# Performance work log

Hardware: AMD Instinct MI355X
Metric: run time of the kernel (lower is better)

Reference implementation:

```python
import jax, jax.numpy as jnp
import numpy as np

D_MODEL = 1024
NUM_HEADS = 16
DEPTH = D_MODEL // NUM_HEADS


def setup_inputs() -> dict:
    key = jax.random.key(0)
    ks = jax.random.split(key, 13)
    B, S = 4, 2048
    s = 1.0 / np.sqrt(D_MODEL)
    return {
        "query": jax.random.normal(ks[0], (B, S, D_MODEL), jnp.float32),
        "key": jax.random.normal(ks[1], (B, S, D_MODEL), jnp.float32),
        "value": jax.random.normal(ks[2], (B, S, D_MODEL), jnp.float32),
        "mask": jax.random.uniform(ks[3], (B, 1, 1, S), jnp.float32),
        "Wq": jax.random.normal(ks[4], (D_MODEL, D_MODEL), jnp.float32) * s,
        "bq": jnp.zeros((D_MODEL,), jnp.float32),
        "Wk": jax.random.normal(ks[5], (D_MODEL, D_MODEL), jnp.float32) * s,
        "bk": jnp.zeros((D_MODEL,), jnp.float32),
        "Wv": jax.random.normal(ks[6], (D_MODEL, D_MODEL), jnp.float32) * s,
        "bv": jnp.zeros((D_MODEL,), jnp.float32),
        "Wo": jax.random.normal(ks[7], (D_MODEL, D_MODEL), jnp.float32) * s,
        "bo": jnp.zeros((D_MODEL,), jnp.float32),
    }


def _split_heads(x):
    # [B, S, d_model] -> [B, H, S, depth]
    B, S, _ = x.shape
    return x.reshape(B, S, NUM_HEADS, DEPTH).transpose(0, 2, 1, 3)


def reference(query, key, value, mask, Wq, bq, Wk, bk, Wv, bv, Wo, bo):
    q = _split_heads(query @ Wq + bq)   # [B,H,Sq,dh]
    k = _split_heads(key @ Wk + bk)     # [B,H,Sk,dh]
    v = _split_heads(value @ Wv + bv)   # [B,H,Sk,dh]
    scale = 1.0 / jnp.sqrt(jnp.float32(DEPTH))
    scores = jnp.einsum("bhqd,bhkd->bhqk", q, k) * scale
    scores = scores + mask * -1e9
    attn = jax.nn.softmax(scores, axis=-1)
    out = jnp.einsum("bhqk,bhkd->bhqd", attn, v)  # [B,H,Sq,dh]
    B, _, Sq, _ = out.shape
    concat = out.transpose(0, 2, 1, 3).reshape(B, Sq, D_MODEL)
    return concat @ Wo + bo
```

## Files before the change

kernel.cpp:

```cpp
#include <hip/hip_runtime.h>

typedef unsigned short ushort_t;
typedef __attribute__((ext_vector_type(8))) short short8;
typedef __attribute__((ext_vector_type(4))) float f32x4;
typedef __attribute__((ext_vector_type(16))) float f32x16;
typedef __attribute__((ext_vector_type(2))) unsigned int uint2v;
typedef __attribute__((ext_vector_type(4))) unsigned int uint4v;
typedef __attribute__((ext_vector_type(2))) unsigned int uint2s;

typedef __attribute__((address_space(1))) const unsigned char gaddr_t;
typedef __attribute__((address_space(3))) unsigned char laddr_t;

__device__ __forceinline__ unsigned short f2bf(float x) {
  unsigned u = __float_as_uint(x);
  u += 0x7FFF + ((u >> 16) & 1);
  return (unsigned short)(u >> 16);
}
__device__ __forceinline__ float bf2f(unsigned short u) {
  return __uint_as_float(((unsigned)u) << 16);
}
__device__ __forceinline__ unsigned cvt_pk_bf16(float lo, float hi) {
  unsigned r;
  asm("v_cvt_pk_bf16_f32 %0, %1, %2" : "=v"(r) : "v"(lo), "v"(hi));
  return r;
}

__device__ __forceinline__ void gl_lds16(const void* g, void* l) {
  __builtin_amdgcn_global_load_lds((gaddr_t*)g, (laddr_t*)l, 16, 0, 0);
}

__device__ __forceinline__ unsigned active_mask(const float* __restrict__ tb) {
  unsigned am = 0;
  float run = -INFINITY;
#pragma unroll
  for (int tt = 0; tt < 32; tt++) {
    float tm = tb[tt];
    if (tm > run - 40.f) am |= (1u << tt);
    run = fmaxf(run, tm);
  }
  return am;
}

__global__ void prep0(const float* __restrict__ maskin, float* __restrict__ maskpre,
                      float* __restrict__ tmaxbuf) {
  const float CM = -1.442695041e9f;
  int bx = blockIdx.x;
  if (bx < 8) {
    int i = bx * 1024 + threadIdx.x * 4;
    f32x4 v = *(const f32x4*)(maskin + i);
    v *= CM;
    *(f32x4*)(maskpre + i) = v;
  } else {
    int t = threadIdx.x;
    if (t < 128) {
      const float* src = maskin + (t >> 5) * 2048 + (t & 31) * 64;
      float mn = src[0];
#pragma unroll
      for (int j = 1; j < 64; j++) mn = fminf(mn, src[j]);
      tmaxbuf[t] = mn * CM;
    }
  }
}

__global__ void prep1(const float4* __restrict__ q4, const float4* __restrict__ k4,
                      const float4* __restrict__ v4,
                      ushort4* __restrict__ xq, ushort4* __restrict__ xk,
                      ushort4* __restrict__ xv,
                      const float* __restrict__ W0, const float* __restrict__ W1,
                      const float* __restrict__ W2, const float* __restrict__ W3,
                      ushort_t* __restrict__ T0, ushort_t* __restrict__ T1,
                      ushort_t* __restrict__ T2, ushort_t* __restrict__ T3,
                      const float* __restrict__ tmaxbuf) {
  const int K = 1024, N = 1024;
  __shared__ ushort_t tile[32][33];
  int bx = blockIdx.x;
  if (bx < 3072) {
    int z = bx >> 10, bl = bx & 1023;
    if (z > 0) {
      int b = bl >> 8, tl = (bl >> 3) & 31;
      unsigned am = active_mask(tmaxbuf + b * 32);
      if (!((am >> tl) & 1u)) return;
    }
    const float4* in = (z == 0) ? q4 : (z == 1) ? k4 : v4;
    ushort4* out = (z == 0) ? xq : (z == 1) ? xk : xv;
    const float4* src = in + (long)bl * 2048;
    ushort4* dst = out + (long)bl * 2048;
    int t = threadIdx.x;
#pragma unroll
    for (int j = 0; j < 8; j++) {
      int idx = j * 256 + t;
      float4 v = src[idx];
      ushort4 o;
      o.x = f2bf(v.x); o.y = f2bf(v.y); o.z = f2bf(v.z); o.w = f2bf(v.w);
      dst[idx] = o;
    }
  } else {
    int idx = bx - 3072;
    int z = idx >> 10;
    const float* W = (z == 0) ? W0 : (z == 1) ? W1 : (z == 2) ? W2 : W3;
    ushort_t* Wt = (z == 0) ? T0 : (z == 1) ? T1 : (z == 2) ? T2 : T3;
    int n0 = (idx & 31) * 32, k0 = ((idx >> 5) & 31) * 32;
    int tx = threadIdx.x & 31, ty = threadIdx.x >> 5;
#pragma unroll
    for (int r = 0; r < 4; r++) {
      int k = k0 + ty + r * 8;
      tile[ty + r * 8][tx] = f2bf(W[(long)k * N + n0 + tx]);
    }
    __syncthreads();
#pragma unroll
    for (int r = 0; r < 4; r++) {
      int n = n0 + ty + r * 8;
      Wt[(long)n * K + k0 + tx] = tile[tx][ty + r * 8];
    }
  }
}

__global__ void gemm_qkv3(
    const ushort_t* __restrict__ Aq, const ushort_t* __restrict__ Ak, const ushort_t* __restrict__ Av,
    const ushort_t* __restrict__ Bq, const ushort_t* __restrict__ Bk, const ushort_t* __restrict__ Bv,
    const float* __restrict__ bq, const float* __restrict__ bk, const float* __restrict__ bv,
    ushort_t* __restrict__ Cq, ushort_t* __restrict__ Ck, ushort_t* __restrict__ Vt,
    const float* __restrict__ tmaxbuf) {
  const int K = 1024, N = 1024;
  const int z = blockIdx.z;
  const ushort_t* A = z == 0 ? Aq : z == 1 ? Ak : Av;
  const ushort_t* Bt = z == 0 ? Bq : z == 1 ? Bk : Bv;
  const float* bias = z == 0 ? bq : z == 1 ? bk : bv;

  __shared__ __align__(16) char smem[49152];
  const int t = threadIdx.x, w = t >> 6, l = t & 63;

  const int orig = blockIdx.x + gridDim.x * blockIdx.y;
  const int xcd = orig & 7, i = orig >> 3;
  const int m0 = (xcd * 8 + (i & 7)) * 128;
  const int n0 = (i >> 3) * 128;
  const int wr = (w >> 1) * 64, wc = (w & 1) * 64;

  if (z != 0) {
    int b_ = m0 >> 11, tile0 = (m0 & 2047) >> 6;
    unsigned am = active_mask(tmaxbuf + b_ * 32);
    if (!((am >> tile0) & 3u)) return;
  }

  f32x4 acc[4][4] = {};

  const int br0 = 16 * w + (l >> 2);
  const int bcs = ((l & 3) ^ ((l >> 3) & 3)) << 3;
  const ushort_t* Ab = A + (long)m0 * K;
  const ushort_t* Bb = Bt + (long)n0 * K;

  auto stage = [&](int kk, int buf) {
    char* base = smem + buf * 16384;
    gl_lds16(Ab + (long)br0 * K + kk + bcs, base + w * 1024);
    gl_lds16(Ab + (long)(br0 + 64) * K + kk + bcs, base + 4096 + w * 1024);
    gl_lds16(Bb + (long)br0 * K + kk + bcs, base + 8192 + w * 1024);
    gl_lds16(Bb + (long)(br0 + 64) * K + kk + bcs, base + 12288 + w * 1024);
  };

  stage(0, 0);
  stage(32, 1);

  const int fsw = ((l >> 4) ^ ((l >> 1) & 3)) << 4;
  const int arow = (wr + (l & 15)) * 64 + fsw;
  const int brow = 8192 + (wc + (l & 15)) * 64 + fsw;

  asm volatile("s_waitcnt vmcnt(4)");
  __builtin_amdgcn_sched_barrier(0);
  __builtin_amdgcn_s_barrier();

  for (int ts = 0; ts < 32; ts++) {
    const char* base = smem + (ts % 3) * 16384;
    if (ts + 2 < 32) stage((ts + 2) * 32, (ts + 2) % 3);
    short8 af[4], bfr[4];
#pragma unroll
    for (int m = 0; m < 4; m++)
      af[m] = *(const short8*)(base + arow + m * 1024);
#pragma unroll
    for (int n = 0; n < 4; n++)
      bfr[n] = *(const short8*)(base + brow + n * 1024);
    __builtin_amdgcn_s_setprio(1);
#pragma unroll
    for (int m = 0; m < 4; m++)
#pragma unroll
      for (int n = 0; n < 4; n++)
        acc[m][n] = __builtin_amdgcn_mfma_f32_16x16x32_bf16(af[m], bfr[n], acc[m][n], 0, 0, 0);
    __builtin_amdgcn_s_setprio(0);
    if (ts < 30) asm volatile("s_waitcnt vmcnt(4)");
    else if (ts == 30) asm volatile("s_waitcnt vmcnt(0)");
    if (ts < 31) {
      __builtin_amdgcn_sched_barrier(0);
      __builtin_amdgcn_s_barrier();
    }
  }
  __builtin_amdgcn_s_barrier();

  char* Lw = smem + w * 8192;
  if (z != 2) {
#pragma unroll
    for (int nn = 0; nn < 4; nn++) {
      float bvv = bias[n0 + wc + nn * 16 + (l & 15)];
      int dl = nn * 16 + (l & 15);
#pragma unroll
      for (int mm = 0; mm < 4; mm++)
#pragma unroll
        for (int i2 = 0; i2 < 4; i2++) {
          int sl = mm * 16 + (l >> 4) * 4 + i2;
          *(ushort_t*)(Lw + sl * 128 + ((dl * 2) ^ ((sl & 7) << 4))) =
              f2bf(acc[mm][nn][i2] + bvv);
        }
    }
    ushort_t* C = (z == 0 ? Cq : Ck) + (long)(m0 + wr) * N + n0 + wc;
#pragma unroll
    for (int rr = 0; rr < 8; rr++) {
      int sl = rr * 8 + (l >> 3);
      short8 vv = *(const short8*)(Lw + sl * 128 + (((l & 7) * 16) ^ ((sl & 7) << 4)));
      *(short8*)(C + (long)sl * N + (l & 7) * 8) = vv;
    }
  } else {
#pragma unroll
    for (int nn = 0; nn < 4; nn++) {
      float bvv = bias[n0 + wc + nn * 16 + (l & 15)];
      int dl = nn * 16 + (l & 15);
#pragma unroll
      for (int mm = 0; mm < 4; mm++) {
        int sl = mm * 16 + (l >> 4) * 4;
        uint2s pk;
        pk.x = cvt_pk_bf16(acc[mm][nn][0] + bvv, acc[mm][nn][1] + bvv);
        pk.y = cvt_pk_bf16(acc[mm][nn][2] + bvv, acc[mm][nn][3] + bvv);
        *(uint2s*)(Lw + dl * 128 + ((sl * 2) ^ ((dl & 7) << 4))) = pk;
      }
    }
    const int b_ = m0 >> 11;
    const int s0g = (m0 & 2047) + wr;
#pragma unroll
    for (int rr = 0; rr < 8; rr++) {
      int dl = rr * 8 + (l >> 3);
      short8 vv = *(const short8*)(Lw + dl * 128 + (((l & 7) * 16) ^ ((dl & 7) << 4)));
      int dg = n0 + wc + dl;
      long rowbase = ((long)(b_ * 16 + (dg >> 6)) * 64 + (dg & 63)) * 2048;
      *(short8*)(Vt + rowbase + s0g + (l & 7) * 8) = vv;
    }
  }
}

__global__ void gemm_o(const ushort_t* __restrict__ A, const ushort_t* __restrict__ Bt,
                       const float* __restrict__ bias, float* __restrict__ C) {
  const int K = 1024, N = 1024;
  __shared__ __align__(16) char smem[49152];
  const int t = threadIdx.x, w = t >> 6, l = t & 63;

  const int orig = blockIdx.x + gridDim.x * blockIdx.y;
  const int xcd = orig & 7, i = orig >> 3;
  const int m0 = (xcd * 8 + (i & 7)) * 128;
  const int n0 = (i >> 3) * 128;
  const int wr = (w >> 1) * 64, wc = (w & 1) * 64;

  f32x4 acc[4][4] = {};

  const int br0 = 16 * w + (l >> 2);
  const int bcs = ((l & 3) ^ ((l >> 3) & 3)) << 3;
  const ushort_t* Ab = A + (long)m0 * K;
  const ushort_t* Bb = Bt + (long)n0 * K;

  auto stage = [&](int kk, int buf) {
    char* base = smem + buf * 16384;
    gl_lds16(Ab + (long)br0 * K + kk + bcs, base + w * 1024);
    gl_lds16(Ab + (long)(br0 + 64) * K + kk + bcs, base + 4096 + w * 1024);
    gl_lds16(Bb + (long)br0 * K + kk + bcs, base + 8192 + w * 1024);
    gl_lds16(Bb + (long)(br0 + 64) * K + kk + bcs, base + 12288 + w * 1024);
  };

  stage(0, 0);
  stage(32, 1);

  const int fsw = ((l >> 4) ^ ((l >> 1) & 3)) << 4;
  const int arow = (wr + (l & 15)) * 64 + fsw;
  const int brow = 8192 + (wc + (l & 15)) * 64 + fsw;

  asm volatile("s_waitcnt vmcnt(4)");
  __builtin_amdgcn_sched_barrier(0);
  __builtin_amdgcn_s_barrier();

  for (int ts = 0; ts < 32; ts++) {
    const char* base = smem + (ts % 3) * 16384;
    if (ts + 2 < 32) stage((ts + 2) * 32, (ts + 2) % 3);
    short8 af[4], bfr[4];
#pragma unroll
    for (int m = 0; m < 4; m++)
      af[m] = *(const short8*)(base + arow + m * 1024);
#pragma unroll
    for (int n = 0; n < 4; n++)
      bfr[n] = *(const short8*)(base + brow + n * 1024);
    __builtin_amdgcn_s_setprio(1);
#pragma unroll
    for (int m = 0; m < 4; m++)
#pragma unroll
      for (int n = 0; n < 4; n++)
        acc[m][n] = __builtin_amdgcn_mfma_f32_16x16x32_bf16(af[m], bfr[n], acc[m][n], 0, 0, 0);
    __builtin_amdgcn_s_setprio(0);
    if (ts < 30) asm volatile("s_waitcnt vmcnt(4)");
    else if (ts == 30) asm volatile("s_waitcnt vmcnt(0)");
    if (ts < 31) {
      __builtin_amdgcn_sched_barrier(0);
      __builtin_amdgcn_s_barrier();
    }
  }

#pragma unroll
  for (int mm = 0; mm < 4; mm++)
#pragma unroll
    for (int nn = 0; nn < 4; nn++) {
      int c = n0 + wc + nn * 16 + (l & 15);
      float bv = bias[c];
#pragma unroll
      for (int i2 = 0; i2 < 4; i2++) {
        int r = m0 + wr + mm * 16 + (l >> 4) * 4 + i2;
        C[(long)r * N + c] = acc[mm][nn][i2] + bv;
      }
    }
}

__global__ __launch_bounds__(256, 4) void attn(
    const ushort_t* __restrict__ Qp, const ushort_t* __restrict__ Kp,
    const ushort_t* __restrict__ Vt, const float* __restrict__ maskpre,
    const float* __restrict__ tmaxbuf, ushort_t* __restrict__ Ob) {
  const int S = 2048, DM = 1024;
  __shared__ __align__(16) char smem[32768];
  char* KlB = smem;
  char* VlB = smem + 16384;

  const int t = threadIdx.x, w = t >> 6, l = t & 63;
  const int lq = l & 31, hi = l >> 5;
  const int hib = hi * 16;

  const int orig = blockIdx.x + (blockIdx.y << 4) + (blockIdx.z << 8);
  const int work = ((orig & 7) << 7) + (orig >> 3);
  const int qx = work & 15;
  const int hb = work >> 4;
  const int h = hb & 15, b = hb >> 4;
  const int q0w = qx * 128 + w * 32;

  const float C1 = 0.1803368801f;

  const ushort_t* Kbase = Kp + (long)(b * S) * DM + h * 64;
  const ushort_t* Vbase = Vt + (long)((b * 16 + h) * 64) * S;
  const float* Mbase = maskpre + (long)b * S;

  short8 qB[4];
  {
    const ushort_t* Qb = Qp + ((long)(b * S) + q0w + lq) * DM + h * 64;
#pragma unroll
    for (int kh = 0; kh < 4; kh++)
      qB[kh] = *(const short8*)(Qb + kh * 16 + hi * 8);
  }

  const int so0 = w * 2048 + l * 16;
  const int sr0 = so0 >> 7, sc0 = (so0 & 127) ^ ((sr0 & 7) << 4);
  const int so1 = so0 + 1024;
  const int sr1 = so1 >> 7, sc1 = (so1 & 127) ^ ((sr1 & 7) << 4);
  const ushort_t* Kg0 = Kbase + (long)sr0 * DM + (sc0 >> 1);
  const ushort_t* Kg1 = Kbase + (long)sr1 * DM + (sc1 >> 1);
  const ushort_t* Vg0 = Vbase + (long)sr0 * S + (sc0 >> 1);
  const ushort_t* Vg1 = Vbase + (long)sr1 * S + (sc1 >> 1);
  char* Kd0 = KlB + w * 2048;
  char* Vd0 = VlB + w * 2048;

  auto stage = [&](int kv0, int bb) {
    long ko = (long)kv0 * DM;
    int bo = bb * 8192;
    gl_lds16(Kg0 + ko, Kd0 + bo);
    gl_lds16(Kg1 + ko, Kd0 + bo + 1024);
    gl_lds16(Vg0 + kv0, Vd0 + bo);
    gl_lds16(Vg1 + kv0, Vd0 + bo + 1024);
  };

  unsigned amask = active_mask(tmaxbuf + b * 32);

  int cur = (int)__builtin_ctz(amask);
  stage(cur * 64, 0);
  __syncthreads();

  const int lbase = lq * 128 + ((lq & 7) << 4);

  f32x16 o0 = {}, o1 = {};
  float mrun = -INFINITY, lsum = 0.f;
  int bb = 0;

  while (cur >= 0) {
    unsigned rem = amask & (0xFFFFFFFEu << cur);
    int nxt = rem ? (int)__builtin_ctz(rem) : -1;
    if (nxt >= 0) stage(nxt * 64, bb ^ 1);
    const int bx = lbase + (bb << 13);
    const int kv0 = cur * 64;

    f32x16 s0 = {}, s1 = {};
    __builtin_amdgcn_s_setprio(1);
#pragma unroll
    for (int kh = 0; kh < 4; kh++) {
      int a = bx ^ (kh * 32 + hib);
      short8 ka0 = *(const short8*)(KlB + a);
      short8 ka1 = *(const short8*)(KlB + a + 4096);
      s0 = __builtin_amdgcn_mfma_f32_32x32x16_bf16(ka0, qB[kh], s0, 0, 0, 0);
      s1 = __builtin_amdgcn_mfma_f32_32x32x16_bf16(ka1, qB[kh], s1, 0, 0, 0);
    }
    __builtin_amdgcn_s_setprio(0);

    const float* mq = Mbase + kv0;
#pragma unroll
    for (int g = 0; g < 4; g++) {
      f32x4 m0 = *(const f32x4*)(mq + g * 8 + hi * 4);
      f32x4 m1 = *(const f32x4*)(mq + 32 + g * 8 + hi * 4);
#pragma unroll
      for (int c = 0; c < 4; c++) {
        s0[g * 4 + c] = fmaf(s0[g * 4 + c], C1, m0[c]);
        s1[g * 4 + c] = fmaf(s1[g * 4 + c], C1, m1[c]);
      }
    }

    float mx0 = -INFINITY, mx1 = -INFINITY, mx2 = -INFINITY, mx3 = -INFINITY;
#pragma unroll
    for (int r = 0; r < 4; r++) {
      mx0 = fmaxf(mx0, fmaxf(s0[r], s0[r + 4]));
      mx1 = fmaxf(mx1, fmaxf(s0[r + 8], s0[r + 12]));
      mx2 = fmaxf(mx2, fmaxf(s1[r], s1[r + 4]));
      mx3 = fmaxf(mx3, fmaxf(s1[r + 8], s1[r + 12]));
    }
    float mx = fmaxf(fmaxf(mx0, mx1), fmaxf(mx2, mx3));
    mx = fmaxf(mx, __shfl_xor(mx, 32));

    if (!__all((int)(mx <= mrun + 8.f))) {
      float mnew = fmaxf(mrun, mx);
      float sc = __builtin_amdgcn_exp2f(mrun - mnew);
      mrun = mnew;
      lsum *= sc;
#pragma unroll
      for (int r = 0; r < 16; r++) { o0[r] *= sc; o1[r] *= sc; }
    }

    float ps0 = 0.f, ps1 = 0.f, ps2 = 0.f, ps3 = 0.f;
#pragma unroll
    for (int r = 0; r < 8; r++) {
      float p0 = __builtin_amdgcn_exp2f(s0[r] - mrun);
      float p1 = __builtin_amdgcn_exp2f(s0[r + 8] - mrun);
      float p2 = __builtin_amdgcn_exp2f(s1[r] - mrun);
      float p3 = __builtin_amdgcn_exp2f(s1[r + 8] - mrun);
      s0[r] = p0; s0[r + 8] = p1; s1[r] = p2; s1[r + 8] = p3;
      ps0 += p0; ps1 += p1; ps2 += p2; ps3 += p3;
    }
    float ps = (ps0 + ps1) + (ps2 + ps3);
    ps += __shfl_xor(ps, 32);
    lsum += ps;

#pragma unroll
    for (int half = 0; half < 2; half++) {
      const f32x16& sv = half ? s1 : s0;
      unsigned x0 = cvt_pk_bf16(sv[0], sv[1]);
      unsigned z0 = cvt_pk_bf16(sv[2], sv[3]);
      unsigned y0 = cvt_pk_bf16(sv[4], sv[5]);
      unsigned u0 = cvt_pk_bf16(sv[6], sv[7]);
      unsigned x1 = cvt_pk_bf16(sv[8], sv[9]);
      unsigned z1 = cvt_pk_bf16(sv[10], sv[11]);
      unsigned y1 = cvt_pk_bf16(sv[12], sv[13]);
      unsigned u1 = cvt_pk_bf16(sv[14], sv[15]);
      uint2v a1 = __builtin_amdgcn_permlane32_swap(x0, y0, false, false);
      uint2v a2 = __builtin_amdgcn_permlane32_swap(z0, u0, false, false);
      uint2v a3 = __builtin_amdgcn_permlane32_swap(x1, y1, false, false);
      uint2v a4 = __builtin_amdgcn_permlane32_swap(z1, u1, false, false);
      uint4v f0, f1;
      f0.x = a1.x; f0.y = a2.x; f0.z = a1.y; f0.w = a2.y;
      f1.x = a3.x; f1.y = a4.x; f1.z = a3.y; f1.w = a4.y;
      short8 pB0 = __builtin_bit_cast(short8, f0);
      short8 pB1 = __builtin_bit_cast(short8, f1);
      __builtin_amdgcn_s_setprio(1);
#pragma unroll
      for (int kt2 = 0; kt2 < 2; kt2++) {
        short8 pB = kt2 ? pB1 : pB0;
        int a = bx ^ (half * 64 + kt2 * 32 + hib);
        short8 va0 = *(const short8*)(VlB + a);
        short8 va1 = *(const short8*)(VlB + a + 4096);
        o0 = __builtin_amdgcn_mfma_f32_32x32x16_bf16(va0, pB, o0, 0, 0, 0);
        o1 = __builtin_amdgcn_mfma_f32_32x32x16_bf16(va1, pB, o1, 0, 0, 0);
      }
      __builtin_amdgcn_s_setprio(0);
    }
    __syncthreads();
    bb ^= 1;
    cur = nxt;
  }

  __syncthreads();
  char* Ow = smem + w * 4096;
  float inv = 1.0f / lsum;
#pragma unroll
  for (int r = 0; r < 16; r++) {
    int d0 = (r & 3) + 8 * (r >> 2) + 4 * hi;
    int a0 = lq * 128 + ((d0 * 2) ^ ((lq & 7) << 4));
    *(ushort_t*)(Ow + a0) = f2bf(o0[r] * inv);
    int d1 = 32 + d0;
    int a1 = lq * 128 + ((d1 * 2) ^ ((lq & 7) << 4));
    *(ushort_t*)(Ow + a1) = f2bf(o1[r] * inv);
  }
  ushort_t* Obase = Ob + ((long)(b * S) + q0w) * DM + h * 64;
#pragma unroll
  for (int rr = 0; rr < 4; rr++) {
    int q = rr * 8 + (l >> 3);
    int a = q * 128 + (((l & 7) * 16) ^ ((q & 7) << 4));
    short8 vv = *(const short8*)(Ow + a);
    *(short8*)(Obase + (long)q * DM + (l & 7) * 8) = vv;
  }
}

extern "C" void kernel_launch(void* const* d_in, const int* in_sizes, int n_in,
                              void* d_out, int out_size, void* d_ws, size_t ws_size,
                              hipStream_t stream) {
  const float* query = (const float*)d_in[0];
  const float* key   = (const float*)d_in[1];
  const float* value = (const float*)d_in[2];
  const float* mask  = (const float*)d_in[3];
  const float* Wq = (const float*)d_in[4];
  const float* bq = (const float*)d_in[5];
  const float* Wk = (const float*)d_in[6];
  const float* bk = (const float*)d_in[7];
  const float* Wv = (const float*)d_in[8];
  const float* bv = (const float*)d_in[9];
  const float* Wo = (const float*)d_in[10];
  const float* bo = (const float*)d_in[11];

  const int B = 4, S = 2048, DM = 1024, H = 16;
  const long M = (long)B * S;
  const long XB = (long)1 << 24;

  char* ws = (char*)d_ws;
  ushort_t* Wqt = (ushort_t*)(ws);
  ushort_t* Wkt = (ushort_t*)(ws + (1l << 21));
  ushort_t* Wvt = (ushort_t*)(ws + 2 * (1l << 21));
  ushort_t* Wot = (ushort_t*)(ws + 3 * (1l << 21));
  ushort_t* Xv  = (ushort_t*)(ws + 4 * (1l << 21));
  ushort_t* Qp  = (ushort_t*)(ws + 4 * (1l << 21) + XB);
  ushort_t* Kp  = Qp + M * DM;
  ushort_t* Vtr = Kp + M * DM;
  float* maskpre = (float*)(Vtr + M * DM);
  float* tmaxbuf = maskpre + (long)B * S;
  ushort_t* AO  = Xv;
  ushort_t* Xq  = (ushort_t*)d_out;
  ushort_t* Xk  = Xq + M * DM;

  prep0<<<9, 256, 0, stream>>>(mask, maskpre, tmaxbuf);

  prep1<<<7168, 256, 0, stream>>>((const float4*)query, (const float4*)key,
                                  (const float4*)value, (ushort4*)Xq, (ushort4*)Xk,
                                  (ushort4*)Xv, Wq, Wk, Wv, Wo, Wqt, Wkt, Wvt, Wot,
                                  tmaxbuf);

  gemm_qkv3<<<dim3(64, 8, 3), 256, 0, stream>>>(Xq, Xk, Xv, Wqt, Wkt, Wvt,
                                                bq, bk, bv, Qp, Kp, Vtr, tmaxbuf);

  attn<<<dim3(16, 16, 4), 256, 0, stream>>>(Qp, Kp, Vtr, maskpre, tmaxbuf, AO);

  gemm_o<<<dim3(64, 8), 256, 0, stream>>>(AO, Wot, bo, (float*)d_out);
}
```

Measured before the change: 130.5 us.

## Enlarge GEMM tiles to 256x256 with 512 threads and 4-stage pipeline

```diff
diff --git a/kernel.cpp b/kernel.cpp
--- a/kernel.cpp
+++ b/kernel.cpp
@@ -115,77 +115,79 @@
   }
 }
 
-__global__ void gemm_qkv3(
+__global__ __launch_bounds__(512, 2) void gemm_qkv3(
     const ushort_t* __restrict__ Aq, const ushort_t* __restrict__ Ak, const ushort_t* __restrict__ Av,
     const ushort_t* __restrict__ Bq, const ushort_t* __restrict__ Bk, const ushort_t* __restrict__ Bv,
     const float* __restrict__ bq, const float* __restrict__ bk, const float* __restrict__ bv,
     ushort_t* __restrict__ Cq, ushort_t* __restrict__ Ck, ushort_t* __restrict__ Vt,
     const float* __restrict__ tmaxbuf) {
   const int K = 1024, N = 1024;
-  const int z = blockIdx.z;
+  const int z = blockIdx.y;
   const ushort_t* A = z == 0 ? Aq : z == 1 ? Ak : Av;
   const ushort_t* Bt = z == 0 ? Bq : z == 1 ? Bk : Bv;
   const float* bias = z == 0 ? bq : z == 1 ? bk : bv;
 
-  __shared__ __align__(16) char smem[49152];
+  __shared__ __align__(16) char smem[131072];
   const int t = threadIdx.x, w = t >> 6, l = t & 63;
 
-  const int orig = blockIdx.x + gridDim.x * blockIdx.y;
+  const int orig = blockIdx.x;
   const int xcd = orig & 7, i = orig >> 3;
-  const int m0 = (xcd * 8 + (i & 7)) * 128;
-  const int n0 = (i >> 3) * 128;
-  const int wr = (w >> 1) * 64, wc = (w & 1) * 64;
+  const int m0 = ((i & 3) * 8 + xcd) * 256;
+  const int n0 = (i >> 2) * 256;
+  const int wr = (w >> 2) * 128, wc = (w & 3) * 64;
 
   if (z != 0) {
     int b_ = m0 >> 11, tile0 = (m0 & 2047) >> 6;
     unsigned am = active_mask(tmaxbuf + b_ * 32);
-    if (!((am >> tile0) & 3u)) return;
-  }
-
-  f32x4 acc[4][4] = {};
-
-  const int br0 = 16 * w + (l >> 2);
+    if (!((am >> tile0) & 15u)) return;
+  }
+
+  f32x4 acc[8][4] = {};
+
+  const int br0 = w * 32 + (l >> 2);
   const int bcs = ((l & 3) ^ ((l >> 3) & 3)) << 3;
   const ushort_t* Ab = A + (long)m0 * K;
   const ushort_t* Bb = Bt + (long)n0 * K;
 
   auto stage = [&](int kk, int buf) {
-    char* base = smem + buf * 16384;
-    gl_lds16(Ab + (long)br0 * K + kk + bcs, base + w * 1024);
-    gl_lds16(Ab + (long)(br0 + 64) * K + kk + bcs, base + 4096 + w * 1024);
-    gl_lds16(Bb + (long)br0 * K + kk + bcs, base + 8192 + w * 1024);
-    gl_lds16(Bb + (long)(br0 + 64) * K + kk + bcs, base + 12288 + w * 1024);
+    char* base = smem + buf * 32768;
+    gl_lds16(Ab + (long)br0 * K + kk + bcs, base + w * 2048);
+    gl_lds16(Ab + (long)(br0 + 16) * K + kk + bcs, base + w * 2048 + 1024);
+    gl_lds16(Bb + (long)br0 * K + kk + bcs, base + 16384 + w * 2048);
+    gl_lds16(Bb + (long)(br0 + 16) * K + kk + bcs, base + 16384 + w * 2048 + 1024);
   };
 
   stage(0, 0);
   stage(32, 1);
+  stage(64, 2);
 
   const int fsw = ((l >> 4) ^ ((l >> 1) & 3)) << 4;
   const int arow = (wr + (l & 15)) * 64 + fsw;
-  const int brow = 8192 + (wc + (l & 15)) * 64 + fsw;
-
-  asm volatile("s_waitcnt vmcnt(4)");
+  const int brow = 16384 + (wc + (l & 15)) * 64 + fsw;
+
+  asm volatile("s_waitcnt vmcnt(8)");
   __builtin_amdgcn_sched_barrier(0);
   __builtin_amdgcn_s_barrier();
 
   for (int ts = 0; ts < 32; ts++) {
-    const char* base = smem + (ts % 3) * 16384;
-    if (ts + 2 < 32) stage((ts + 2) * 32, (ts + 2) % 3);
-    short8 af[4], bfr[4];
-#pragma unroll
-    for (int m = 0; m < 4; m++)
+    const char* base = smem + (ts & 3) * 32768;
+    if (ts + 3 < 32) stage((ts + 3) * 32, (ts + 3) & 3);
+    short8 af[8], bfr[4];
+#pragma unroll
+    for (int m = 0; m < 8; m++)
       af[m] = *(const short8*)(base + arow + m * 1024);
 #pragma unroll
     for (int n = 0; n < 4; n++)
       bfr[n] = *(const short8*)(base + brow + n * 1024);
     __builtin_amdgcn_s_setprio(1);
 #pragma unroll
-    for (int m = 0; m < 4; m++)
+    for (int m = 0; m < 8; m++)
 #pragma unroll
       for (int n = 0; n < 4; n++)
         acc[m][n] = __builtin_amdgcn_mfma_f32_16x16x32_bf16(af[m], bfr[n], acc[m][n], 0, 0, 0);
     __builtin_amdgcn_s_setprio(0);
-    if (ts < 30) asm volatile("s_waitcnt vmcnt(4)");
+    if (ts < 29) asm volatile("s_waitcnt vmcnt(8)");
+    else if (ts == 29) asm volatile("s_waitcnt vmcnt(4)");
     else if (ts == 30) asm volatile("s_waitcnt vmcnt(0)");
     if (ts < 31) {
       __builtin_amdgcn_sched_barrier(0);
@@ -194,14 +196,14 @@
   }
   __builtin_amdgcn_s_barrier();
 
-  char* Lw = smem + w * 8192;
+  char* Lw = smem + w * 16384;
   if (z != 2) {
 #pragma unroll
     for (int nn = 0; nn < 4; nn++) {
       float bvv = bias[n0 + wc + nn * 16 + (l & 15)];
       int dl = nn * 16 + (l & 15);
 #pragma unroll
-      for (int mm = 0; mm < 4; mm++)
+      for (int mm = 0; mm < 8; mm++)
 #pragma unroll
         for (int i2 = 0; i2 < 4; i2++) {
           int sl = mm * 16 + (l >> 4) * 4 + i2;
@@ -211,7 +213,7 @@
     }
     ushort_t* C = (z == 0 ? Cq : Ck) + (long)(m0 + wr) * N + n0 + wc;
 #pragma unroll
-    for (int rr = 0; rr < 8; rr++) {
+    for (int rr = 0; rr < 16; rr++) {
       int sl = rr * 8 + (l >> 3);
       short8 vv = *(const short8*)(Lw + sl * 128 + (((l & 7) * 16) ^ ((sl & 7) << 4)));
       *(short8*)(C + (long)sl * N + (l & 7) * 8) = vv;
@@ -222,12 +224,12 @@
       float bvv = bias[n0 + wc + nn * 16 + (l & 15)];
       int dl = nn * 16 + (l & 15);
 #pragma unroll
-      for (int mm = 0; mm < 4; mm++) {
+      for (int mm = 0; mm < 8; mm++) {
         int sl = mm * 16 + (l >> 4) * 4;
         uint2s pk;
         pk.x = cvt_pk_bf16(acc[mm][nn][0] + bvv, acc[mm][nn][1] + bvv);
         pk.y = cvt_pk_bf16(acc[mm][nn][2] + bvv, acc[mm][nn][3] + bvv);
-        *(uint2s*)(Lw + dl * 128 + ((sl * 2) ^ ((dl & 7) << 4))) = pk;
+        *(uint2s*)(Lw + dl * 256 + ((sl * 2) ^ ((dl & 7) << 4))) = pk;
       }
     }
     const int b_ = m0 >> 11;
@@ -235,70 +237,78 @@
 #pragma unroll
     for (int rr = 0; rr < 8; rr++) {
       int dl = rr * 8 + (l >> 3);
-      short8 vv = *(const short8*)(Lw + dl * 128 + (((l & 7) * 16) ^ ((dl & 7) << 4)));
       int dg = n0 + wc + dl;
       long rowbase = ((long)(b_ * 16 + (dg >> 6)) * 64 + (dg & 63)) * 2048;
-      *(short8*)(Vt + rowbase + s0g + (l & 7) * 8) = vv;
-    }
-  }
-}
-
-__global__ void gemm_o(const ushort_t* __restrict__ A, const ushort_t* __restrict__ Bt,
-                       const float* __restrict__ bias, float* __restrict__ C) {
+#pragma unroll
+      for (int sh = 0; sh < 2; sh++) {
+        int c = (l & 7) + sh * 8;
+        short8 vv = *(const short8*)(Lw + dl * 256 + ((c * 16) ^ ((dl & 7) << 4)));
+        *(short8*)(Vt + rowbase + s0g + c * 8) = vv;
+      }
+    }
+  }
+}
+
+__global__ __launch_bounds__(512, 2) void gemm_o(const ushort_t* __restrict__ A,
+                                                 const ushort_t* __restrict__ Bt,
+                                                 const float* __restrict__ bias,
+                                                 float* __restrict__ C) {
   const int K = 1024, N = 1024;
-  __shared__ __align__(16) char smem[49152];
+  __shared__ __align__(16) char smem[131072];
   const int t = threadIdx.x, w = t >> 6, l = t & 63;
 
-  const int orig = blockIdx.x + gridDim.x * blockIdx.y;
+  const int orig = blockIdx.x;
   const int xcd = orig & 7, i = orig >> 3;
-  const int m0 = (xcd * 8 + (i & 7)) * 128;
-  const int n0 = (i >> 3) * 128;
-  const int wr = (w >> 1) * 64, wc = (w & 1) * 64;
-
-  f32x4 acc[4][4] = {};
-
-  const int br0 = 16 * w + (l >> 2);
+  const int m0 = ((i & 3) * 8 + xcd) * 256;
+  const int n0 = (i >> 2) * 256;
+  const int wr = (w >> 2) * 128, wc = (w & 3) * 64;
+
+  f32x4 acc[8][4] = {};
+
+  const int br0 = w * 32 + (l >> 2);
   const int bcs = ((l & 3) ^ ((l >> 3) & 3)) << 3;
   const ushort_t* Ab = A + (long)m0 * K;
   const ushort_t* Bb = Bt + (long)n0 * K;
 
   auto stage = [&](int kk, int buf) {
-    char* base = smem + buf * 16384;
-    gl_lds16(Ab + (long)br0 * K + kk + bcs, base + w * 1024);
-    gl_lds16(Ab + (long)(br0 + 64) * K + kk + bcs, base + 4096 + w * 1024);
-    gl_lds16(Bb + (long)br0 * K + kk + bcs, base + 8192 + w * 1024);
-    gl_lds16(Bb + (long)(br0 + 64) * K + kk + bcs, base + 12288 + w * 1024);
+    char* base = smem + buf * 32768;
+    gl_lds16(Ab + (long)br0 * K + kk + bcs, base + w * 2048);
+    gl_lds16(Ab + (long)(br0 + 16) * K + kk + bcs, base + w * 2048 + 1024);
+    gl_lds16(Bb + (long)br0 * K + kk + bcs, base + 16384 + w * 2048);
+    gl_lds16(Bb + (long)(br0 + 16) * K + kk + bcs, base + 16384 + w * 2048 + 1024);
   };
 
   stage(0, 0);
   stage(32, 1);
+  stage(64, 2);
 
   const int fsw = ((l >> 4) ^ ((l >> 1) & 3)) << 4;
   const int arow = (wr + (l & 15)) * 64 + fsw;
-  const int brow = 8192 + (wc + (l & 15)) * 64 + fsw;
-
-  asm volatile("s_waitcnt vmcnt(4)");
+  const int brow = 16384 + (wc + (l & 15)) * 64 + fsw;
+
+  asm volatile("s_waitcnt vmcnt(8)");
   __builtin_amdgcn_sched_barrier(0);
   __builtin_amdgcn_s_barrier();
 
   for (int ts = 0; ts < 32; ts++) {
-    const char* base = smem + (ts % 3) * 16384;
-    if (ts + 2 < 32) stage((ts + 2) * 32, (ts + 2) % 3);
-    short8 af[4], bfr[4];
-#pragma unroll
-    for (int m = 0; m < 4; m++)
+    const char* base = smem + (ts & 3) * 32768;
+    if (ts + 3 < 32) stage((ts + 3) * 32, (ts + 3) & 3);
+    short8 af[8], bfr[4];
+#pragma unroll
+    for (int m = 0; m < 8; m++)
       af[m] = *(const short8*)(base + arow + m * 1024);
 #pragma unroll
     for (int n = 0; n < 4; n++)
       bfr[n] = *(const short8*)(base + brow + n * 1024);
     __builtin_amdgcn_s_setprio(1);
 #pragma unroll
-    for (int m = 0; m < 4; m++)
+    for (int m = 0; m < 8; m++)
 #pragma unroll
       for (int n = 0; n < 4; n++)
         acc[m][n] = __builtin_amdgcn_mfma_f32_16x16x32_bf16(af[m], bfr[n], acc[m][n], 0, 0, 0);
     __builtin_amdgcn_s_setprio(0);
-    if (ts < 30) asm volatile("s_waitcnt vmcnt(4)");
+    if (ts < 29) asm volatile("s_waitcnt vmcnt(8)");
+    else if (ts == 29) asm volatile("s_waitcnt vmcnt(4)");
     else if (ts == 30) asm volatile("s_waitcnt vmcnt(0)");
     if (ts < 31) {
       __builtin_amdgcn_sched_barrier(0);
@@ -307,7 +317,7 @@
   }
 
 #pragma unroll
-  for (int mm = 0; mm < 4; mm++)
+  for (int mm = 0; mm < 8; mm++)
 #pragma unroll
     for (int nn = 0; nn < 4; nn++) {
       int c = n0 + wc + nn * 16 + (l & 15);
@@ -552,10 +562,10 @@
                                   (ushort4*)Xv, Wq, Wk, Wv, Wo, Wqt, Wkt, Wvt, Wot,
                                   tmaxbuf);
 
-  gemm_qkv3<<<dim3(64, 8, 3), 256, 0, stream>>>(Xq, Xk, Xv, Wqt, Wkt, Wvt,
-                                                bq, bk, bv, Qp, Kp, Vtr, tmaxbuf);
+  gemm_qkv3<<<dim3(128, 3), 512, 0, stream>>>(Xq, Xk, Xv, Wqt, Wkt, Wvt,
+                                              bq, bk, bv, Qp, Kp, Vtr, tmaxbuf);
 
   attn<<<dim3(16, 16, 4), 256, 0, stream>>>(Qp, Kp, Vtr, maskpre, tmaxbuf, AO);
 
-  gemm_o<<<dim3(64, 8), 256, 0, stream>>>(AO, Wot, bo, (float*)d_out);
-}
+  gemm_o<<<128, 512, 0, stream>>>(AO, Wot, bo, (float*)d_out);
+}
```

Result: slower. 147.7 us (+13.2%).

## Fuse fp32-to-bf16 activation conversion into QKV GEMM LDS load path

Applied to the files above, without the earlier changes.

```diff
diff --git a/kernel.cpp b/kernel.cpp
--- a/kernel.cpp
+++ b/kernel.cpp
@@ -62,72 +62,44 @@
   }
 }
 
-__global__ void prep1(const float4* __restrict__ q4, const float4* __restrict__ k4,
-                      const float4* __restrict__ v4,
-                      ushort4* __restrict__ xq, ushort4* __restrict__ xk,
-                      ushort4* __restrict__ xv,
-                      const float* __restrict__ W0, const float* __restrict__ W1,
-                      const float* __restrict__ W2, const float* __restrict__ W3,
-                      ushort_t* __restrict__ T0, ushort_t* __restrict__ T1,
-                      ushort_t* __restrict__ T2, ushort_t* __restrict__ T3,
-                      const float* __restrict__ tmaxbuf) {
+__global__ void prep1w(const float* __restrict__ W0, const float* __restrict__ W1,
+                       const float* __restrict__ W2, const float* __restrict__ W3,
+                       ushort_t* __restrict__ T0, ushort_t* __restrict__ T1,
+                       ushort_t* __restrict__ T2, ushort_t* __restrict__ T3) {
   const int K = 1024, N = 1024;
   __shared__ ushort_t tile[32][33];
-  int bx = blockIdx.x;
-  if (bx < 3072) {
-    int z = bx >> 10, bl = bx & 1023;
-    if (z > 0) {
-      int b = bl >> 8, tl = (bl >> 3) & 31;
-      unsigned am = active_mask(tmaxbuf + b * 32);
-      if (!((am >> tl) & 1u)) return;
-    }
-    const float4* in = (z == 0) ? q4 : (z == 1) ? k4 : v4;
-    ushort4* out = (z == 0) ? xq : (z == 1) ? xk : xv;
-    const float4* src = in + (long)bl * 2048;
-    ushort4* dst = out + (long)bl * 2048;
-    int t = threadIdx.x;
-#pragma unroll
-    for (int j = 0; j < 8; j++) {
-      int idx = j * 256 + t;
-      float4 v = src[idx];
-      ushort4 o;
-      o.x = f2bf(v.x); o.y = f2bf(v.y); o.z = f2bf(v.z); o.w = f2bf(v.w);
-      dst[idx] = o;
-    }
-  } else {
-    int idx = bx - 3072;
-    int z = idx >> 10;
-    const float* W = (z == 0) ? W0 : (z == 1) ? W1 : (z == 2) ? W2 : W3;
-    ushort_t* Wt = (z == 0) ? T0 : (z == 1) ? T1 : (z == 2) ? T2 : T3;
-    int n0 = (idx & 31) * 32, k0 = ((idx >> 5) & 31) * 32;
-    int tx = threadIdx.x & 31, ty = threadIdx.x >> 5;
-#pragma unroll
-    for (int r = 0; r < 4; r++) {
-      int k = k0 + ty + r * 8;
-      tile[ty + r * 8][tx] = f2bf(W[(long)k * N + n0 + tx]);
-    }
-    __syncthreads();
-#pragma unroll
-    for (int r = 0; r < 4; r++) {
-      int n = n0 + ty + r * 8;
-      Wt[(long)n * K + k0 + tx] = tile[tx][ty + r * 8];
-    }
+  int idx = blockIdx.x;
+  int z = idx >> 10;
+  const float* W = (z == 0) ? W0 : (z == 1) ? W1 : (z == 2) ? W2 : W3;
+  ushort_t* Wt = (z == 0) ? T0 : (z == 1) ? T1 : (z == 2) ? T2 : T3;
+  int n0 = (idx & 31) * 32, k0 = ((idx >> 5) & 31) * 32;
+  int tx = threadIdx.x & 31, ty = threadIdx.x >> 5;
+#pragma unroll
+  for (int r = 0; r < 4; r++) {
+    int k = k0 + ty + r * 8;
+    tile[ty + r * 8][tx] = f2bf(W[(long)k * N + n0 + tx]);
+  }
+  __syncthreads();
+#pragma unroll
+  for (int r = 0; r < 4; r++) {
+    int n = n0 + ty + r * 8;
+    Wt[(long)n * K + k0 + tx] = tile[tx][ty + r * 8];
   }
 }
 
 __global__ void gemm_qkv3(
-    const ushort_t* __restrict__ Aq, const ushort_t* __restrict__ Ak, const ushort_t* __restrict__ Av,
+    const float* __restrict__ Aq, const float* __restrict__ Ak, const float* __restrict__ Av,
     const ushort_t* __restrict__ Bq, const ushort_t* __restrict__ Bk, const ushort_t* __restrict__ Bv,
     const float* __restrict__ bq, const float* __restrict__ bk, const float* __restrict__ bv,
     ushort_t* __restrict__ Cq, ushort_t* __restrict__ Ck, ushort_t* __restrict__ Vt,
     const float* __restrict__ tmaxbuf) {
   const int K = 1024, N = 1024;
   const int z = blockIdx.z;
-  const ushort_t* A = z == 0 ? Aq : z == 1 ? Ak : Av;
+  const float* A = z == 0 ? Aq : z == 1 ? Ak : Av;
   const ushort_t* Bt = z == 0 ? Bq : z == 1 ? Bk : Bv;
   const float* bias = z == 0 ? bq : z == 1 ? bk : bv;
 
-  __shared__ __align__(16) char smem[49152];
+  __shared__ __align__(16) char smem[73728];
   const int t = threadIdx.x, w = t >> 6, l = t & 63;
 
   const int orig = blockIdx.x + gridDim.x * blockIdx.y;
@@ -144,37 +116,52 @@
 
   f32x4 acc[4][4] = {};
 
+  const long aswzsrc = (long)(((l & 7) ^ (l >> 3)) * 4);
+  const float* Am = A + (long)m0 * K;
   const int br0 = 16 * w + (l >> 2);
   const int bcs = ((l & 3) ^ ((l >> 3) & 3)) << 3;
-  const ushort_t* Ab = A + (long)m0 * K;
   const ushort_t* Bb = Bt + (long)n0 * K;
 
-  auto stage = [&](int kk, int buf) {
-    char* base = smem + buf * 16384;
-    gl_lds16(Ab + (long)br0 * K + kk + bcs, base + w * 1024);
-    gl_lds16(Ab + (long)(br0 + 64) * K + kk + bcs, base + 4096 + w * 1024);
-    gl_lds16(Bb + (long)br0 * K + kk + bcs, base + 8192 + w * 1024);
-    gl_lds16(Bb + (long)(br0 + 64) * K + kk + bcs, base + 12288 + w * 1024);
+  auto stage = [&](int ks, int buf) {
+    char* ab = smem + buf * 24576;
+    char* bb2 = ab + 16384;
+    const float* As = Am + ks * 32 + aswzsrc;
+#pragma unroll
+    for (int c = 0; c < 4; c++)
+      gl_lds16(As + (long)(c * 32 + w * 8 + (l >> 3)) * K, ab + c * 4096 + w * 1024);
+    const ushort_t* Bs = Bb + ks * 32 + bcs;
+    gl_lds16(Bs + (long)br0 * K, bb2 + w * 1024);
+    gl_lds16(Bs + (long)(br0 + 64) * K, bb2 + 4096 + w * 1024);
   };
 
   stage(0, 0);
-  stage(32, 1);
-
+  stage(1, 1);
+
+  const int arA = (wr + (l & 15)) * 128;
+  const int aswz0 = ((2 * (l >> 4)) ^ (l & 7)) << 4;
+  const int aswz1 = ((2 * (l >> 4) + 1) ^ (l & 7)) << 4;
   const int fsw = ((l >> 4) ^ ((l >> 1) & 3)) << 4;
-  const int arow = (wr + (l & 15)) * 64 + fsw;
-  const int brow = 8192 + (wc + (l & 15)) * 64 + fsw;
-
-  asm volatile("s_waitcnt vmcnt(4)");
+  const int brow = 16384 + (wc + (l & 15)) * 64 + fsw;
+
+  asm volatile("s_waitcnt vmcnt(6)");
   __builtin_amdgcn_sched_barrier(0);
   __builtin_amdgcn_s_barrier();
 
   for (int ts = 0; ts < 32; ts++) {
-    const char* base = smem + (ts % 3) * 16384;
-    if (ts + 2 < 32) stage((ts + 2) * 32, (ts + 2) % 3);
+    const char* base = smem + (ts % 3) * 24576;
+    if (ts + 2 < 32) stage(ts + 2, (ts + 2) % 3);
     short8 af[4], bfr[4];
 #pragma unroll
-    for (int m = 0; m < 4; m++)
-      af[m] = *(const short8*)(base + arow + m * 1024);
+    for (int m = 0; m < 4; m++) {
+      f32x4 lo = *(const f32x4*)(base + arA + m * 2048 + aswz0);
+      f32x4 hi = *(const f32x4*)(base + arA + m * 2048 + aswz1);
+      uint4v up;
+      up.x = cvt_pk_bf16(lo[0], lo[1]);
+      up.y = cvt_pk_bf16(lo[2], lo[3]);
+      up.z = cvt_pk_bf16(hi[0], hi[1]);
+      up.w = cvt_pk_bf16(hi[2], hi[3]);
+      af[m] = __builtin_bit_cast(short8, up);
+    }
 #pragma unroll
     for (int n = 0; n < 4; n++)
       bfr[n] = *(const short8*)(base + brow + n * 1024);
@@ -185,7 +172,7 @@
       for (int n = 0; n < 4; n++)
         acc[m][n] = __builtin_amdgcn_mfma_f32_16x16x32_bf16(af[m], bfr[n], acc[m][n], 0, 0, 0);
     __builtin_amdgcn_s_setprio(0);
-    if (ts < 30) asm volatile("s_waitcnt vmcnt(4)");
+    if (ts < 30) asm volatile("s_waitcnt vmcnt(6)");
     else if (ts == 30) asm volatile("s_waitcnt vmcnt(0)");
     if (ts < 31) {
       __builtin_amdgcn_sched_barrier(0);
@@ -535,24 +522,18 @@
   ushort_t* Wkt = (ushort_t*)(ws + (1l << 21));
   ushort_t* Wvt = (ushort_t*)(ws + 2 * (1l << 21));
   ushort_t* Wot = (ushort_t*)(ws + 3 * (1l << 21));
-  ushort_t* Xv  = (ushort_t*)(ws + 4 * (1l << 21));
+  ushort_t* AO  = (ushort_t*)(ws + 4 * (1l << 21));
   ushort_t* Qp  = (ushort_t*)(ws + 4 * (1l << 21) + XB);
   ushort_t* Kp  = Qp + M * DM;
   ushort_t* Vtr = Kp + M * DM;
   float* maskpre = (float*)(Vtr + M * DM);
   float* tmaxbuf = maskpre + (long)B * S;
-  ushort_t* AO  = Xv;
-  ushort_t* Xq  = (ushort_t*)d_out;
-  ushort_t* Xk  = Xq + M * DM;
 
   prep0<<<9, 256, 0, stream>>>(mask, maskpre, tmaxbuf);
 
-  prep1<<<7168, 256, 0, stream>>>((const float4*)query, (const float4*)key,
-                                  (const float4*)value, (ushort4*)Xq, (ushort4*)Xk,
-                                  (ushort4*)Xv, Wq, Wk, Wv, Wo, Wqt, Wkt, Wvt, Wot,
-                                  tmaxbuf);
-
-  gemm_qkv3<<<dim3(64, 8, 3), 256, 0, stream>>>(Xq, Xk, Xv, Wqt, Wkt, Wvt,
+  prep1w<<<4096, 256, 0, stream>>>(Wq, Wk, Wv, Wo, Wqt, Wkt, Wvt, Wot);
+
+  gemm_qkv3<<<dim3(64, 8, 3), 256, 0, stream>>>(query, key, value, Wqt, Wkt, Wvt,
                                                 bq, bk, bv, Qp, Kp, Vtr, tmaxbuf);
 
   attn<<<dim3(16, 16, 4), 256, 0, stream>>>(Qp, Kp, Vtr, maskpre, tmaxbuf, AO);
```

Result: slower. 138.1 us (+5.9%).
